# Performance work log

Hardware: AMD Instinct MI355X
Metric: run time of the kernel (lower is better)

Reference implementation:

```python
import jax, jax.numpy as jnp
import numpy as np

P, S, IMG = 8, 4, 256          # patch_size, stride, img_size
HID, GH, B = 64, 128, 4        # conv hidden ch, gcn hidden ch, batch
Ph = (IMG - P) // S + 1        # 63 patches per side
N = Ph * Ph                    # 3969 patch-nodes


def _conv(x, w, b):
    y = jax.lax.conv_general_dilated(x, w, (1, 1), 'SAME',
                                     dimension_numbers=('NCHW', 'OIHW', 'NCHW'))
    return y + b[None, :, None, None]


def _img2patch(x):
    # x: [B,1,H,W] -> [B, N, P*P] (row-major patch pixels, matching torch reshape)
    pt = jax.lax.conv_general_dilated_patches(x, (P, P), (S, S), 'VALID')  # [B, P*P, Ph, Pw]
    b = x.shape[0]
    return pt.reshape(b, P * P, N).transpose(0, 2, 1)


def _patch2img(y):
    # y: [b, N, P*P] -> [b, 1, IMG, IMG] via overlap scatter-add
    b = y.shape[0]
    y = y.reshape(b, Ph, Ph, P, P)
    x = jnp.zeros((b, 1, IMG, IMG), y.dtype)
    hi = S * (Ph - 1) + 1
    for i in range(P):          # fixed small loop over patch pixels (64 iters)
        for j in range(P):
            x = x.at[:, 0, i:i + hi:S, j:j + hi:S].add(y[:, :, :, i, j])
    return x


def _gcn(x, adj, w, bias):
    # x: [B,N,F_in], adj: [B,N,N] -> [B,N,F_out]
    support = jnp.einsum('bnf,fg->bng', x, w)
    return jnp.einsum('bnm,bmg->bng', adj, support) + bias


def setup_inputs() -> dict:
    key = jax.random.key(0)
    ks = jax.random.split(key, 14)
    sc = 0.05
    return {
        'input_data': jax.random.normal(ks[0], (B, 1, IMG, IMG), jnp.float32),
        'proj': jax.random.normal(ks[1], (B, 1, IMG, IMG), jnp.float32),
        'adj': jax.random.uniform(ks[2], (B, N, N), jnp.float32) / N,
        'lam': jnp.float32(0.5),
        'conv_w1': jax.random.normal(ks[3], (HID, 1, 3, 3), jnp.float32) * sc,
        'conv_b1': jnp.zeros((HID,), jnp.float32),
        'conv_w2': jax.random.normal(ks[4], (HID, HID, 3, 3), jnp.float32) * sc,
        'conv_b2': jnp.zeros((HID,), jnp.float32),
        'conv_w3': jax.random.normal(ks[5], (1, HID, 3, 3), jnp.float32) * sc,
        'conv_b3': jnp.zeros((1,), jnp.float32),
        'gcn_w3': jax.random.normal(ks[6], (P * P, GH), jnp.float32) * sc,
        'gcn_b3': jnp.zeros((GH,), jnp.float32),
        'gcn_w4': jax.random.normal(ks[7], (GH, P * P), jnp.float32) * sc,
        'gcn_b4': jnp.zeros((P * P,), jnp.float32),
    }


def reference(input_data, proj, adj, lam,
              conv_w1, conv_b1, conv_w2, conv_b2, conv_w3, conv_b3,
              gcn_w3, gcn_b3, gcn_w4, gcn_b4):
    # block1: data-fidelity step (fidelity_module modeled as DC update)
    tmp1 = input_data + lam * (proj - input_data)
    # block2: 3-layer CNN
    h = jax.nn.relu(_conv(input_data, conv_w1, conv_b1))
    h = jax.nn.relu(_conv(h, conv_w2, conv_b2))
    tmp2 = _conv(h, conv_w3, conv_b3)
    # block3/4: patch-graph GCN branch
    patch = _img2patch(input_data)                 # [B, N, P*P]
    g = jax.nn.relu(_gcn(patch, adj, gcn_w3, gcn_b3))
    g = _gcn(g, adj, gcn_w4, gcn_b4)               # [B, N, P*P]
    # Patch2Im with overlap-count normalization mask
    mask = _patch2img(jnp.ones((1, N, P * P), jnp.float32))
    tmp3 = _patch2img(g) / mask
    return jax.nn.relu(tmp1 + tmp2 + tmp3)
```

## Files before the change

kernel.cpp:

```cpp
#include <hip/hip_runtime.h>

#define IMG   256
#define NPIX  65536
#define PH    63
#define NNODE 3969
#define SN    4000
#define HID   64
#define GH    128
#define BATCH 4

typedef __attribute__((ext_vector_type(8))) short short8;
typedef __attribute__((ext_vector_type(4))) float float4v;
typedef unsigned short ushort_t;

__device__ inline ushort_t f2bf(float f) {
    union { float f; unsigned u; } v; v.f = f;
    unsigned r = v.u + 0x7FFF + ((v.u >> 16) & 1);
    return (ushort_t)(r >> 16);
}

__global__ __launch_bounds__(256) void k_cvt_adj(const float* __restrict__ adj,
                                                 ushort_t* __restrict__ adjb) {
    int n = blockIdx.x, b = blockIdx.y;
    const float* src = adj + (size_t)(b * NNODE + n) * NNODE;
    unsigned* dst = (unsigned*)(adjb + (size_t)(b * NNODE + n) * SN);
    for (int c2 = threadIdx.x; c2 < SN / 2; c2 += 256) {
        int c = c2 * 2;
        float f0 = (c < NNODE) ? src[c] : 0.f;
        float f1 = (c + 1 < NNODE) ? src[c + 1] : 0.f;
        dst[c2] = (unsigned)f2bf(f0) | ((unsigned)f2bf(f1) << 16);
    }
}

__global__ __launch_bounds__(256) void k_sup1(const float* __restrict__ in,
                                              const float* __restrict__ w3,
                                              ushort_t* __restrict__ sup1T) {
    int b = blockIdx.z;
    int g = blockIdx.y * 8 + (threadIdx.x >> 5);
    int n = blockIdx.x * 32 + (threadIdx.x & 31);
    ushort_t* dst = sup1T + (size_t)b * GH * SN + (size_t)g * SN + n;
    if (n >= NNODE) { *dst = 0; return; }
    int py = n / PH, px = n - py * PH;
    const float* base = in + (size_t)b * NPIX + (py * 4) * IMG + px * 4;
    float acc = 0.f;
#pragma unroll
    for (int i = 0; i < 8; ++i)
#pragma unroll
        for (int j = 0; j < 8; ++j)
            acc += base[i * IMG + j] * w3[(i * 8 + j) * GH + g];
    *dst = f2bf(acc);
}

template <int G>
__global__ __launch_bounds__(256) void k_gemm_mfma(const ushort_t* __restrict__ adjb,
                                                   const ushort_t* __restrict__ supT,
                                                   float* __restrict__ C) {
    constexpr int FN = (G == 128) ? 4 : 2;
    const int b = blockIdx.z, ks = blockIdx.y;
    const int node0 = blockIdx.x * 128;
    const int t = threadIdx.x;
    const int lane = t & 63, w = t >> 6;
    const int l15 = lane & 15, q = lane >> 4;
    const int wm0 = (G == 128) ? (w & 1) * 64 : 0;
    const int wn0 = (G == 128) ? (w >> 1) * 64 : w * 32;

    __shared__ ushort_t Als[G][40];
    __shared__ ushort_t Bls[128][40];

    const int k0c = ks * 992;
    const int kend = (ks == 3) ? NNODE : k0c + 992;
    const int kiters = (kend - k0c + 31) >> 5;

    const ushort_t* Ab = supT + (size_t)b * G * SN;
    const ushort_t* Bb = adjb + (size_t)b * NNODE * SN;
    float* Cb = C + (size_t)b * G * SN;

    float4v acc[4][FN];
#pragma unroll
    for (int i = 0; i < 4; ++i)
#pragma unroll
        for (int j = 0; j < FN; ++j)
#pragma unroll
            for (int r = 0; r < 4; ++r) acc[i][j][r] = 0.f;

    for (int kk = 0; kk < kiters; ++kk) {
        const int kbase = k0c + kk * 32;
#pragma unroll
        for (int i = 0; i < G / 64; ++i) {
            int idx = t + i * 256;
            int r = idx >> 2, s = idx & 3;
            *(uint4*)&Als[r][s * 8] =
                *(const uint4*)&Ab[(size_t)r * SN + kbase + s * 8];
        }
#pragma unroll
        for (int i = 0; i < 2; ++i) {
            int idx = t + i * 256;
            int r = idx >> 2, s = idx & 3;
            *(uint4*)&Bls[r][s * 8] =
                *(const uint4*)&Bb[(size_t)(node0 + r) * SN + kbase + s * 8];
        }
        __syncthreads();
        short8 af[4], bf[FN];
#pragma unroll
        for (int i = 0; i < 4; ++i)
            af[i] = *(const short8*)&Als[wm0 + i * 16 + l15][q * 8];
#pragma unroll
        for (int j = 0; j < FN; ++j)
            bf[j] = *(const short8*)&Bls[wn0 + j * 16 + l15][q * 8];
#pragma unroll
        for (int i = 0; i < 4; ++i)
#pragma unroll
            for (int j = 0; j < FN; ++j)
                acc[i][j] = __builtin_amdgcn_mfma_f32_16x16x32_bf16(
                    af[i], bf[j], acc[i][j], 0, 0, 0);
        __syncthreads();
    }
#pragma unroll
    for (int i = 0; i < 4; ++i) {
        int gg = wm0 + i * 16 + q * 4;
#pragma unroll
        for (int j = 0; j < FN; ++j) {
            int nn = node0 + wn0 + j * 16 + l15;
            if (nn < NNODE) {
#pragma unroll
                for (int r = 0; r < 4; ++r)
                    unsafeAtomicAdd(&Cb[(size_t)(gg + r) * SN + nn], acc[i][j][r]);
            }
        }
    }
}

__global__ __launch_bounds__(256) void k_sup2(const float* __restrict__ g1T,
                                              const float* __restrict__ gb3,
                                              const float* __restrict__ w4,
                                              ushort_t* __restrict__ sup2T) {
    int b = blockIdx.z;
    int g = blockIdx.y * 8 + (threadIdx.x >> 5);
    int n = blockIdx.x * 32 + (threadIdx.x & 31);
    const float* gb = g1T + (size_t)b * GH * SN + n;
    float acc = 0.f;
#pragma unroll 8
    for (int k = 0; k < GH; ++k) {
        float v = fmaxf(gb[(size_t)k * SN] + gb3[k], 0.f);
        acc += v * w4[k * 64 + g];
    }
    sup2T[(size_t)b * 64 * SN + (size_t)g * SN + n] = (n < NNODE) ? f2bf(acc) : 0;
}

__global__ __launch_bounds__(256) void k_conv1(const float* __restrict__ in,
                                               const float* __restrict__ w,
                                               const float* __restrict__ bias,
                                               ushort_t* __restrict__ h1n) {
    int b = blockIdx.z;
    const float* inb = in + (size_t)b * NPIX;
    __shared__ float s[18][18];
    __shared__ float ws[576];
    int tx = threadIdx.x & 15, ty = threadIdx.x >> 4;
    int x0 = blockIdx.x * 16, y0 = blockIdx.y * 16;
    for (int idx = threadIdx.x; idx < 324; idx += 256) {
        int yy = idx / 18, xx = idx - yy * 18;
        int gy = y0 + yy - 1, gx = x0 + xx - 1;
        s[yy][xx] = (gy >= 0 && gy < IMG && gx >= 0 && gx < IMG) ? inb[gy * IMG + gx] : 0.f;
    }
    for (int idx = threadIdx.x; idx < 576; idx += 256) ws[idx] = w[idx];
    __syncthreads();
    float r[9];
#pragma unroll
    for (int dy = 0; dy < 3; ++dy)
#pragma unroll
        for (int dx = 0; dx < 3; ++dx) r[dy * 3 + dx] = s[ty + dy][tx + dx];
    int outp = (y0 + ty) * IMG + x0 + tx;
    ushort_t* dst = h1n + ((size_t)b * NPIX + outp) * 64;
#pragma unroll
    for (int sgrp = 0; sgrp < 8; ++sgrp) {
        unsigned pk[4];
#pragma unroll
        for (int h = 0; h < 4; ++h) {
            int oc0 = sgrp * 8 + h * 2;
            float a0 = bias[oc0], a1 = bias[oc0 + 1];
#pragma unroll
            for (int k = 0; k < 9; ++k) {
                a0 += r[k] * ws[oc0 * 9 + k];
                a1 += r[k] * ws[(oc0 + 1) * 9 + k];
            }
            a0 = fmaxf(a0, 0.f); a1 = fmaxf(a1, 0.f);
            pk[h] = (unsigned)f2bf(a0) | ((unsigned)f2bf(a1) << 16);
        }
        *(uint4*)&dst[sgrp * 8] = *(uint4*)pk;
    }
}

__global__ __launch_bounds__(256) void k_prepack(const float* __restrict__ w,
                                                 ushort_t* __restrict__ W2p) {
    int idx = blockIdx.x * 256 + threadIdx.x;
    if (idx >= 36864) return;
    int tap = idx >> 12, rem = idx & 4095;
    int oc = rem >> 6, ic = rem & 63;
    W2p[idx] = f2bf(w[(oc * 64 + ic) * 9 + tap]);
}

__global__ __launch_bounds__(256) void k_conv2(const ushort_t* __restrict__ h1n,
                                               const ushort_t* __restrict__ W2p,
                                               const float* __restrict__ bias,
                                               float* __restrict__ h2) {
    __shared__ ushort_t Xs[340 * 72];
    const int b = blockIdx.z;
    const ushort_t* h1b = h1n + (size_t)b * NPIX * 64;
    float* h2b = h2 + (size_t)b * 64 * NPIX;
    const int t = threadIdx.x;
    const int lane = t & 63, w = t >> 6;
    const int l15 = lane & 15, q = lane >> 4;
    const int x0 = blockIdx.x * 32, y0 = blockIdx.y * 8;

    for (int idx = t; idx < 2720; idx += 256) {
        int hp = idx >> 3, s = idx & 7;
        int hy = hp / 34, hx = hp - hy * 34;
        int gy = y0 + hy - 1, gx = x0 + hx - 1;
        uint4 v = {0u, 0u, 0u, 0u};
        if (gy >= 0 && gy < IMG && gx >= 0 && gx < IMG)
            v = *(const uint4*)&h1b[((size_t)gy * IMG + gx) * 64 + s * 8];
        *(uint4*)&Xs[hp * 72 + s * 8] = v;
    }
    __syncthreads();

    const int wn0 = w * 64;
    int pbase[4];
#pragma unroll
    for (int j = 0; j < 4; ++j) {
        int p = wn0 + j * 16 + l15;
        pbase[j] = (p >> 5) * 34 + (p & 31);
    }

    float4v acc[4][4];
#pragma unroll
    for (int i = 0; i < 4; ++i)
#pragma unroll
        for (int j = 0; j < 4; ++j)
#pragma unroll
            for (int r = 0; r < 4; ++r) acc[i][j][r] = 0.f;

    for (int tap = 0; tap < 9; ++tap) {
        int ky = tap / 3, kx = tap - ky * 3;
        const ushort_t* wp = W2p + tap * 4096;
#pragma unroll
        for (int c = 0; c < 2; ++c) {
            short8 af[4], bf[4];
#pragma unroll
            for (int i = 0; i < 4; ++i)
                af[i] = *(const short8*)&wp[(i * 16 + l15) * 64 + c * 32 + q * 8];
#pragma unroll
            for (int j = 0; j < 4; ++j)
                bf[j] = *(const short8*)&Xs[(pbase[j] + ky * 34 + kx) * 72 + c * 32 + q * 8];
#pragma unroll
            for (int i = 0; i < 4; ++i)
#pragma unroll
                for (int j = 0; j < 4; ++j)
                    acc[i][j] = __builtin_amdgcn_mfma_f32_16x16x32_bf16(
                        af[i], bf[j], acc[i][j], 0, 0, 0);
        }
    }

#pragma unroll
    for (int i = 0; i < 4; ++i) {
#pragma unroll
        for (int j = 0; j < 4; ++j) {
            int p = wn0 + j * 16 + l15;
            int y = y0 + (p >> 5), x = x0 + (p & 31);
#pragma unroll
            for (int r = 0; r < 4; ++r) {
                int oc = i * 16 + q * 4 + r;
                h2b[(size_t)oc * NPIX + (size_t)y * IMG + x] =
                    fmaxf(acc[i][j][r] + bias[oc], 0.f);
            }
        }
    }
}

__global__ __launch_bounds__(256) void k_combine(const float* __restrict__ in,
                                                 const float* __restrict__ proj,
                                                 const float* __restrict__ lamp,
                                                 const float* __restrict__ h2,
                                                 const float* __restrict__ wc,
                                                 const float* __restrict__ bc,
                                                 const float* __restrict__ g2T,
                                                 const float* __restrict__ gb4,
                                                 float* __restrict__ out) {
    int b = blockIdx.z;
    const float* inb = in + (size_t)b * NPIX;
    const float* prb = proj + (size_t)b * NPIX;
    const float* h2b = h2 + (size_t)b * 64 * NPIX;
    const float* g2b = g2T + (size_t)b * 64 * SN;
    __shared__ float s[16][18][18];
    __shared__ float ws[144];
    int tx = threadIdx.x & 15, ty = threadIdx.x >> 4;
    int x0 = blockIdx.x * 16, y0 = blockIdx.y * 16;
    int y = y0 + ty, x = x0 + tx;

    float acc = bc[0];
    for (int icc = 0; icc < 4; ++icc) {
        for (int idx = threadIdx.x; idx < 16 * 324; idx += 256) {
            int ic = idx / 324, rem = idx - ic * 324;
            int yy = rem / 18, xx = rem - yy * 18;
            int gy = y0 + yy - 1, gx = x0 + xx - 1;
            s[ic][yy][xx] = (gy >= 0 && gy < IMG && gx >= 0 && gx < IMG)
                                ? h2b[(icc * 16 + ic) * NPIX + gy * IMG + gx]
                                : 0.f;
        }
        for (int idx = threadIdx.x; idx < 144; idx += 256) ws[idx] = wc[icc * 144 + idx];
        __syncthreads();
#pragma unroll 4
        for (int ic = 0; ic < 16; ++ic) {
#pragma unroll
            for (int ky = 0; ky < 3; ++ky)
#pragma unroll
                for (int kx = 0; kx < 3; ++kx)
                    acc += s[ic][ty + ky][tx + kx] * ws[ic * 9 + ky * 3 + kx];
        }
        __syncthreads();
    }

    float iv = inb[y * IMG + x], pv = prb[y * IMG + x];
    float tmp1 = iv + lamp[0] * (pv - iv);

    int pylo = (y >= 4) ? ((y - 4) >> 2) : 0;
    int pyhi = min(62, y >> 2);
    int pxlo = (x >= 4) ? ((x - 4) >> 2) : 0;
    int pxhi = min(62, x >> 2);
    float sum = 0.f;
    int cnt = 0;
    for (int py = pylo; py <= pyhi; ++py)
        for (int px = pxlo; px <= pxhi; ++px) {
            int pix = (y - 4 * py) * 8 + (x - 4 * px);
            sum += g2b[(size_t)pix * SN + (py * PH + px)] + gb4[pix];
            ++cnt;
        }
    float tmp3 = sum / (float)cnt;

    out[(size_t)b * NPIX + y * IMG + x] = fmaxf(tmp1 + acc + tmp3, 0.f);
}

extern "C" void kernel_launch(void* const* d_in, const int* in_sizes, int n_in,
                              void* d_out, int out_size, void* d_ws, size_t ws_size,
                              hipStream_t stream) {
    const float* input = (const float*)d_in[0];
    const float* proj  = (const float*)d_in[1];
    const float* adj   = (const float*)d_in[2];
    const float* lam   = (const float*)d_in[3];
    const float* cw1   = (const float*)d_in[4];
    const float* cb1   = (const float*)d_in[5];
    const float* cw2   = (const float*)d_in[6];
    const float* cb2   = (const float*)d_in[7];
    const float* cw3   = (const float*)d_in[8];
    const float* cb3   = (const float*)d_in[9];
    const float* gw3   = (const float*)d_in[10];
    const float* gb3   = (const float*)d_in[11];
    const float* gw4   = (const float*)d_in[12];
    const float* gb4   = (const float*)d_in[13];
    float* out = (float*)d_out;

    char* base = (char*)d_ws;
    float*    g2T   = (float*)base;
    char*     pool  = base + 4096000;
    ushort_t* adjb  = (ushort_t*)pool;
    ushort_t* sup1T = (ushort_t*)(pool + 127008000);
    float*    g1T   = (float*)(pool + 127008000 + 4096000);
    ushort_t* sup2T = (ushort_t*)(pool + 127008000 + 4096000 + 8192000);
    ushort_t* h1n   = (ushort_t*)pool;
    float*    h2    = (float*)(pool + 33554432);
    ushort_t* W2p   = (ushort_t*)(pool + 33554432 + 67108864);

    dim3 blk(256);

    hipMemsetAsync(g1T, 0, 8192000, stream);
    hipMemsetAsync(g2T, 0, 4096000, stream);

    k_cvt_adj<<<dim3(NNODE, BATCH), blk, 0, stream>>>(adj, adjb);
    k_sup1<<<dim3(125, 16, BATCH), blk, 0, stream>>>(input, gw3, sup1T);
    k_gemm_mfma<128><<<dim3(32, 4, BATCH), blk, 0, stream>>>(adjb, sup1T, g1T);
    k_sup2<<<dim3(125, 8, BATCH), blk, 0, stream>>>(g1T, gb3, gw4, sup2T);
    k_gemm_mfma<64><<<dim3(32, 4, BATCH), blk, 0, stream>>>(adjb, sup2T, g2T);

    k_prepack<<<dim3(144), blk, 0, stream>>>(cw2, W2p);
    k_conv1<<<dim3(16, 16, BATCH), blk, 0, stream>>>(input, cw1, cb1, h1n);
    k_conv2<<<dim3(8, 32, BATCH), blk, 0, stream>>>(h1n, W2p, cb2, h2);
    k_combine<<<dim3(16, 16, BATCH), blk, 0, stream>>>(
        input, proj, lam, h2, cw3, cb3, g2T, gb4, out);
}
```

Before: 701.7 us.

## Move GCN feature projections onto bf16 MFMA with transposed intermediate layout

Replaces the scalar per-thread sup1 and sup2 projections with MFMA bf16 GEMM kernels that use pre-packed bf16 weights. The first big GEMM now writes its output node-major so a new activation kernel can produce contiguous bf16 rows for the second projection. Weight packing is merged into one prepack kernel. This adds a kernel launch and bf16 rounding of the projection inputs, and the transposed atomic writes may change contention patterns. The workspace layout is also reorganised and no longer aliases buffers.

```diff
diff --git a/kernel.cpp b/kernel.cpp
--- a/kernel.cpp
+++ b/kernel.cpp
@@ -5,6 +5,7 @@
 #define PH    63
 #define NNODE 3969
 #define SN    4000
+#define SN2   4096
 #define HID   64
 #define GH    128
 #define BATCH 4
@@ -17,6 +18,9 @@
     union { float f; unsigned u; } v; v.f = f;
     unsigned r = v.u + 0x7FFF + ((v.u >> 16) & 1);
     return (ushort_t)(r >> 16);
+}
+__device__ inline unsigned pk2(float a, float b) {
+    return (unsigned)f2bf(a) | ((unsigned)f2bf(b) << 16);
 }
 
 __global__ __launch_bounds__(256) void k_cvt_adj(const float* __restrict__ adj,
@@ -28,30 +32,100 @@
         int c = c2 * 2;
         float f0 = (c < NNODE) ? src[c] : 0.f;
         float f1 = (c + 1 < NNODE) ? src[c + 1] : 0.f;
-        dst[c2] = (unsigned)f2bf(f0) | ((unsigned)f2bf(f1) << 16);
+        dst[c2] = pk2(f0, f1);
+    }
+}
+
+__global__ __launch_bounds__(256) void k_prepack(const float* __restrict__ cw2,
+                                                 const float* __restrict__ w3,
+                                                 const float* __restrict__ w4,
+                                                 ushort_t* __restrict__ W2p,
+                                                 ushort_t* __restrict__ w3p,
+                                                 ushort_t* __restrict__ w4p) {
+    int idx = blockIdx.x * 256 + threadIdx.x;
+    if (idx < 36864) {
+        int tap = idx >> 12, rem = idx & 4095;
+        int oc = rem >> 6, ic = rem & 63;
+        W2p[idx] = f2bf(cw2[(oc * 64 + ic) * 9 + tap]);
+    } else if (idx < 45056) {
+        int i2 = idx - 36864;
+        int g = i2 >> 6, pix = i2 & 63;
+        w3p[i2] = f2bf(w3[pix * GH + g]);
+    } else if (idx < 53248) {
+        int i3 = idx - 45056;
+        int g = i3 >> 7, k = i3 & 127;
+        w4p[i3] = f2bf(w4[k * 64 + g]);
     }
 }
 
 __global__ __launch_bounds__(256) void k_sup1(const float* __restrict__ in,
-                                              const float* __restrict__ w3,
+                                              const ushort_t* __restrict__ w3p,
                                               ushort_t* __restrict__ sup1T) {
-    int b = blockIdx.z;
-    int g = blockIdx.y * 8 + (threadIdx.x >> 5);
-    int n = blockIdx.x * 32 + (threadIdx.x & 31);
-    ushort_t* dst = sup1T + (size_t)b * GH * SN + (size_t)g * SN + n;
-    if (n >= NNODE) { *dst = 0; return; }
-    int py = n / PH, px = n - py * PH;
-    const float* base = in + (size_t)b * NPIX + (py * 4) * IMG + px * 4;
-    float acc = 0.f;
-#pragma unroll
-    for (int i = 0; i < 8; ++i)
-#pragma unroll
-        for (int j = 0; j < 8; ++j)
-            acc += base[i * IMG + j] * w3[(i * 8 + j) * GH + g];
-    *dst = f2bf(acc);
-}
-
-template <int G>
+    __shared__ ushort_t Ps[128][72];
+    const int b = blockIdx.z;
+    const int n0 = blockIdx.x * 128;
+    const float* inb = in + (size_t)b * NPIX;
+    const int t = threadIdx.x;
+    const int lane = t & 63, w = t >> 6;
+    const int l15 = lane & 15, q = lane >> 4;
+
+    for (int idx = t; idx < 1024; idx += 256) {
+        int nl = idx >> 3, i = idx & 7;
+        int n = n0 + nl;
+        unsigned pk[4] = {0u, 0u, 0u, 0u};
+        if (n < NNODE) {
+            int py = n / PH, px = n - py * PH;
+            const float* rp = inb + (py * 4 + i) * IMG + px * 4;
+            float4 a = *(const float4*)rp;
+            float4 c = *(const float4*)(rp + 4);
+            pk[0] = pk2(a.x, a.y); pk[1] = pk2(a.z, a.w);
+            pk[2] = pk2(c.x, c.y); pk[3] = pk2(c.z, c.w);
+        }
+        *(uint4*)&Ps[nl][i * 8] = *(uint4*)pk;
+    }
+    __syncthreads();
+
+    const int g0 = (w & 1) * 64, nw = (w >> 1) * 64;
+    float4v acc[4][4];
+#pragma unroll
+    for (int i = 0; i < 4; ++i)
+#pragma unroll
+        for (int j = 0; j < 4; ++j)
+#pragma unroll
+            for (int r = 0; r < 4; ++r) acc[i][j][r] = 0.f;
+
+#pragma unroll
+    for (int c = 0; c < 2; ++c) {
+        short8 af[4], bf[4];
+#pragma unroll
+        for (int i = 0; i < 4; ++i)
+            af[i] = *(const short8*)&w3p[(g0 + i * 16 + l15) * 64 + c * 32 + q * 8];
+#pragma unroll
+        for (int j = 0; j < 4; ++j)
+            bf[j] = *(const short8*)&Ps[nw + j * 16 + l15][c * 32 + q * 8];
+#pragma unroll
+        for (int i = 0; i < 4; ++i)
+#pragma unroll
+            for (int j = 0; j < 4; ++j)
+                acc[i][j] = __builtin_amdgcn_mfma_f32_16x16x32_bf16(
+                    af[i], bf[j], acc[i][j], 0, 0, 0);
+    }
+    ushort_t* dst = sup1T + (size_t)b * GH * SN;
+#pragma unroll
+    for (int i = 0; i < 4; ++i)
+#pragma unroll
+        for (int j = 0; j < 4; ++j) {
+            int n = n0 + nw + j * 16 + l15;
+            if (n < SN) {
+                int g = g0 + i * 16 + q * 4;
+#pragma unroll
+                for (int r = 0; r < 4; ++r)
+                    dst[(size_t)(g + r) * SN + n] = f2bf(acc[i][j][r]);
+            }
+        }
+}
+
+template <int G, bool TRANS>
 __global__ __launch_bounds__(256) void k_gemm_mfma(const ushort_t* __restrict__ adjb,
                                                    const ushort_t* __restrict__ supT,
                                                    float* __restrict__ C) {
@@ -73,7 +147,6 @@
 
     const ushort_t* Ab = supT + (size_t)b * G * SN;
     const ushort_t* Bb = adjb + (size_t)b * NNODE * SN;
-    float* Cb = C + (size_t)b * G * SN;
 
     float4v acc[4][FN];
 #pragma unroll
@@ -115,36 +188,114 @@
                     af[i], bf[j], acc[i][j], 0, 0, 0);
         __syncthreads();
     }
-#pragma unroll
-    for (int i = 0; i < 4; ++i) {
-        int gg = wm0 + i * 16 + q * 4;
-#pragma unroll
-        for (int j = 0; j < FN; ++j) {
-            int nn = node0 + wn0 + j * 16 + l15;
-            if (nn < NNODE) {
+    if (TRANS) {
+        float* Cb = C + (size_t)b * SN2 * 128;
+#pragma unroll
+        for (int i = 0; i < 4; ++i) {
+            int gg = wm0 + i * 16 + q * 4;
+#pragma unroll
+            for (int j = 0; j < FN; ++j) {
+                int nn = node0 + wn0 + j * 16 + l15;
+                if (nn < NNODE) {
+#pragma unroll
+                    for (int r = 0; r < 4; ++r)
+                        unsafeAtomicAdd(&Cb[(size_t)nn * 128 + gg + r], acc[i][j][r]);
+                }
+            }
+        }
+    } else {
+        float* Cb = C + (size_t)b * G * SN;
+#pragma unroll
+        for (int i = 0; i < 4; ++i) {
+            int gg = wm0 + i * 16 + q * 4;
+#pragma unroll
+            for (int j = 0; j < FN; ++j) {
+                int nn = node0 + wn0 + j * 16 + l15;
+                if (nn < NNODE) {
+#pragma unroll
+                    for (int r = 0; r < 4; ++r)
+                        unsafeAtomicAdd(&Cb[(size_t)(gg + r) * SN + nn], acc[i][j][r]);
+                }
+            }
+        }
+    }
+}
+
+__global__ __launch_bounds__(256) void k_act(const float* __restrict__ g1n,
+                                             const float* __restrict__ gb3,
+                                             ushort_t* __restrict__ a1t) {
+    int idx = blockIdx.x * 256 + threadIdx.x;
+    int b = idx >> 16, rem = idx & 65535;
+    int n = rem >> 4, kg = rem & 15;
+    const float* src = g1n + ((size_t)b * SN2 + n) * 128 + kg * 8;
+    float4 a = *(const float4*)src;
+    float4 c = *(const float4*)(src + 4);
+    float4 ba = *(const float4*)(gb3 + kg * 8);
+    float4 bc = *(const float4*)(gb3 + kg * 8 + 4);
+    unsigned pk[4];
+    pk[0] = pk2(fmaxf(a.x + ba.x, 0.f), fmaxf(a.y + ba.y, 0.f));
+    pk[1] = pk2(fmaxf(a.z + ba.z, 0.f), fmaxf(a.w + ba.w, 0.f));
+    pk[2] = pk2(fmaxf(c.x + bc.x, 0.f), fmaxf(c.y + bc.y, 0.f));
+    pk[3] = pk2(fmaxf(c.z + bc.z, 0.f), fmaxf(c.w + bc.w, 0.f));
+    *(uint4*)(a1t + ((size_t)b * SN2 + n) * 128 + kg * 8) = *(uint4*)pk;
+}
+
+__global__ __launch_bounds__(256) void k_gemm_s2(const ushort_t* __restrict__ a1t,
+                                                 const ushort_t* __restrict__ w4p,
+                                                 ushort_t* __restrict__ sup2T) {
+    __shared__ ushort_t Ls[128][136];
+    const int b = blockIdx.y;
+    const int n0 = blockIdx.x * 128;
+    const int t = threadIdx.x;
+    const int lane = t & 63, w = t >> 6;
+    const int l15 = lane & 15, q = lane >> 4;
+
+    const ushort_t* src = a1t + (size_t)b * SN2 * 128;
+    for (int idx = t; idx < 2048; idx += 256) {
+        int nl = idx >> 4, kg = idx & 15;
+        *(uint4*)&Ls[nl][kg * 8] =
+            *(const uint4*)&src[(size_t)(n0 + nl) * 128 + kg * 8];
+    }
+    __syncthreads();
+
+    const int nw = w * 32;
+    float4v acc[4][2];
+#pragma unroll
+    for (int i = 0; i < 4; ++i)
+#pragma unroll
+        for (int j = 0; j < 2; ++j)
+#pragma unroll
+            for (int r = 0; r < 4; ++r) acc[i][j][r] = 0.f;
+
+#pragma unroll
+    for (int c = 0; c < 4; ++c) {
+        short8 af[4], bf[2];
+#pragma unroll
+        for (int i = 0; i < 4; ++i)
+            af[i] = *(const short8*)&w4p[(i * 16 + l15) * 128 + c * 32 + q * 8];
+#pragma unroll
+        for (int j = 0; j < 2; ++j)
+            bf[j] = *(const short8*)&Ls[nw + j * 16 + l15][c * 32 + q * 8];
+#pragma unroll
+        for (int i = 0; i < 4; ++i)
+#pragma unroll
+            for (int j = 0; j < 2; ++j)
+                acc[i][j] = __builtin_amdgcn_mfma_f32_16x16x32_bf16(
+                    af[i], bf[j], acc[i][j], 0, 0, 0);
+    }
+    ushort_t* dst = sup2T + (size_t)b * 64 * SN;
+#pragma unroll
+    for (int i = 0; i < 4; ++i)
+#pragma unroll
+        for (int j = 0; j < 2; ++j) {
+            int n = n0 + nw + j * 16 + l15;
+            if (n < SN) {
+                int g = i * 16 + q * 4;
 #pragma unroll
                 for (int r = 0; r < 4; ++r)
-                    unsafeAtomicAdd(&Cb[(size_t)(gg + r) * SN + nn], acc[i][j][r]);
+                    dst[(size_t)(g + r) * SN + n] = f2bf(acc[i][j][r]);
             }
         }
-    }
-}
-
-__global__ __launch_bounds__(256) void k_sup2(const float* __restrict__ g1T,
-                                              const float* __restrict__ gb3,
-                                              const float* __restrict__ w4,
-                                              ushort_t* __restrict__ sup2T) {
-    int b = blockIdx.z;
-    int g = blockIdx.y * 8 + (threadIdx.x >> 5);
-    int n = blockIdx.x * 32 + (threadIdx.x & 31);
-    const float* gb = g1T + (size_t)b * GH * SN + n;
-    float acc = 0.f;
-#pragma unroll 8
-    for (int k = 0; k < GH; ++k) {
-        float v = fmaxf(gb[(size_t)k * SN] + gb3[k], 0.f);
-        acc += v * w4[k * 64 + g];
-    }
-    sup2T[(size_t)b * 64 * SN + (size_t)g * SN + n] = (n < NNODE) ? f2bf(acc) : 0;
 }
 
 __global__ __launch_bounds__(256) void k_conv1(const float* __restrict__ in,
@@ -183,20 +334,10 @@
                 a0 += r[k] * ws[oc0 * 9 + k];
                 a1 += r[k] * ws[(oc0 + 1) * 9 + k];
             }
-            a0 = fmaxf(a0, 0.f); a1 = fmaxf(a1, 0.f);
-            pk[h] = (unsigned)f2bf(a0) | ((unsigned)f2bf(a1) << 16);
+            pk[h] = pk2(fmaxf(a0, 0.f), fmaxf(a1, 0.f));
         }
         *(uint4*)&dst[sgrp * 8] = *(uint4*)pk;
     }
-}
-
-__global__ __launch_bounds__(256) void k_prepack(const float* __restrict__ w,
-                                                 ushort_t* __restrict__ W2p) {
-    int idx = blockIdx.x * 256 + threadIdx.x;
-    if (idx >= 36864) return;
-    int tap = idx >> 12, rem = idx & 4095;
-    int oc = rem >> 6, ic = rem & 63;
-    W2p[idx] = f2bf(w[(oc * 64 + ic) * 9 + tap]);
 }
 
 __global__ __launch_bounds__(256) void k_conv2(const ushort_t* __restrict__ h1n,
@@ -259,7 +400,6 @@
                         af[i], bf[j], acc[i][j], 0, 0, 0);
         }
     }
-
 #pragma unroll
     for (int i = 0; i < 4; ++i) {
 #pragma unroll
@@ -359,28 +499,32 @@
     float* out = (float*)d_out;
 
     char* base = (char*)d_ws;
-    float*    g2T   = (float*)base;
-    char*     pool  = base + 4096000;
-    ushort_t* adjb  = (ushort_t*)pool;
-    ushort_t* sup1T = (ushort_t*)(pool + 127008000);
-    float*    g1T   = (float*)(pool + 127008000 + 4096000);
-    ushort_t* sup2T = (ushort_t*)(pool + 127008000 + 4096000 + 8192000);
-    ushort_t* h1n   = (ushort_t*)pool;
-    float*    h2    = (float*)(pool + 33554432);
-    ushort_t* W2p   = (ushort_t*)(pool + 33554432 + 67108864);
+    float*    g2T   = (float*)(base);
+    ushort_t* adjb  = (ushort_t*)(base + 4096000);
+    ushort_t* sup1T = (ushort_t*)(base + 131104000);
+    float*    g1n   = (float*)(base + 135200000);
+    ushort_t* a1t   = (ushort_t*)(base + 143588608);
+    ushort_t* sup2T = (ushort_t*)(base + 147782912);
+    ushort_t* w3p   = (ushort_t*)(base + 149830912);
+    ushort_t* w4p   = (ushort_t*)(base + 149847296);
+    ushort_t* W2p   = (ushort_t*)(base + 149863680);
+    ushort_t* h1n   = (ushort_t*)(base + 149937408);
+    float*    h2    = (float*)(base + 183491840);
 
     dim3 blk(256);
 
-    hipMemsetAsync(g1T, 0, 8192000, stream);
-    hipMemsetAsync(g2T, 0, 4096000, stream);
-
+    hipMemsetAsync(g1n, 0, (size_t)BATCH * SN2 * 128 * 4, stream);
+    hipMemsetAsync(g2T, 0, (size_t)BATCH * 64 * SN * 4, stream);
+
+    k_prepack<<<dim3(208), blk, 0, stream>>>(cw2, gw3, gw4, W2p, w3p, w4p);
     k_cvt_adj<<<dim3(NNODE, BATCH), blk, 0, stream>>>(adj, adjb);
-    k_sup1<<<dim3(125, 16, BATCH), blk, 0, stream>>>(input, gw3, sup1T);
-    k_gemm_mfma<128><<<dim3(32, 4, BATCH), blk, 0, stream>>>(adjb, sup1T, g1T);
-    k_sup2<<<dim3(125, 8, BATCH), blk, 0, stream>>>(g1T, gb3, gw4, sup2T);
-    k_gemm_mfma<64><<<dim3(32, 4, BATCH), blk, 0, stream>>>(adjb, sup2T, g2T);
-
-    k_prepack<<<dim3(144), blk, 0, stream>>>(cw2, W2p);
+
+    k_sup1<<<dim3(32, 1, BATCH), blk, 0, stream>>>(input, w3p, sup1T);
+    k_gemm_mfma<128, true><<<dim3(32, 4, BATCH), blk, 0, stream>>>(adjb, sup1T, g1n);
+    k_act<<<dim3(1024), blk, 0, stream>>>(g1n, gb3, a1t);
+    k_gemm_s2<<<dim3(32, BATCH), blk, 0, stream>>>(a1t, w4p, sup2T);
+    k_gemm_mfma<64, false><<<dim3(32, 4, BATCH), blk, 0, stream>>>(adjb, sup2T, g2T);
+
     k_conv1<<<dim3(16, 16, BATCH), blk, 0, stream>>>(input, cw1, cb1, h1n);
     k_conv2<<<dim3(8, 32, BATCH), blk, 0, stream>>>(h1n, W2p, cb2, h2);
     k_combine<<<dim3(16, 16, BATCH), blk, 0, stream>>>(
```

Measured after the change: 719.7 us. +2.6%, slower.
